# Optimization experiments

Hardware: AMD Instinct MI355X
Metric: run time of the kernel (lower is better)

Reference implementation:

```python
import jax, jax.numpy as jnp
import numpy as np
import math

D_MODEL = 1024
NUM_HEADS = 16
HEAD_DIM = D_MODEL // NUM_HEADS


def setup_inputs() -> dict:
    key = jax.random.key(0)
    ks = jax.random.split(key, 10)
    B, Sq, Skv = 2, 2048, 2048
    s = 1.0 / math.sqrt(D_MODEL)
    return {
        "X": jax.random.normal(ks[0], (B, Skv, D_MODEL), jnp.float32),
        "y": jax.random.normal(ks[1], (B, Sq, D_MODEL), jnp.float32),
        "qW": jax.random.normal(ks[2], (D_MODEL, D_MODEL), jnp.float32) * s,
        "qB": jnp.zeros((D_MODEL,), jnp.float32),
        "kW": jax.random.normal(ks[3], (D_MODEL, D_MODEL), jnp.float32) * s,
        "kB": jnp.zeros((D_MODEL,), jnp.float32),
        "vW": jax.random.normal(ks[4], (D_MODEL, D_MODEL), jnp.float32) * s,
        "vB": jnp.zeros((D_MODEL,), jnp.float32),
        "oW": jax.random.normal(ks[5], (D_MODEL, D_MODEL), jnp.float32) * s,
        "oB": jnp.zeros((D_MODEL,), jnp.float32),
    }


def _split_heads(x):
    # (B, S, D) -> (B, H, S, dk)
    B, S, _ = x.shape
    return x.reshape(B, S, NUM_HEADS, HEAD_DIM).transpose(0, 2, 1, 3)


def reference(X, y, qW, qB, kW, kB, vW, vB, oW, oB):
    B = X.shape[0]
    q = _split_heads(y @ qW + qB)   # queries come from y (decoder)
    k = _split_heads(X @ kW + kB)   # keys/values from X (encoder)
    v = _split_heads(X @ vW + vB)
    scale = 1.0 / math.sqrt(HEAD_DIM)
    scores = jnp.einsum("bhqd,bhkd->bhqk", q, k) * scale
    weights = jax.nn.softmax(scores, axis=-1)
    attn = jnp.einsum("bhqk,bhkd->bhqd", weights, v)
    concat = attn.transpose(0, 2, 1, 3).reshape(B, -1, D_MODEL)
    return concat @ oW + oB
```

## Files before the change

kernel.cpp:

```cpp
#include <hip/hip_runtime.h>
#include <hip/hip_bf16.h>
#include <math.h>

typedef __hip_bfloat16 bf16;
typedef __bf16 nbf16;
typedef __bf16 bf16x8 __attribute__((ext_vector_type(8)));
typedef __bf16 bf16x4 __attribute__((ext_vector_type(4)));
typedef float f32x4 __attribute__((ext_vector_type(4)));

#define D_MODEL 1024
#define NHEAD   16
#define HDK     64
#define BATCH   2
#define SEQ     2048
#define QSZ     ((size_t)BATCH * SEQ * D_MODEL)
#define WSZ     ((size_t)D_MODEL * D_MODEL)

__global__ void detect_dtype(const unsigned short* __restrict__ x, int* flag) {
    __shared__ int cnt;
    if (threadIdx.x == 0) cnt = 0;
    __syncthreads();
    int local = 0;
    for (int i = threadIdx.x; i < 4096; i += 256) {
        const unsigned short v = x[i];
        const int e = (v >> 7) & 0xFF;
        if (v == 0 || (e >= 96 && e <= 141)) local++;
    }
    atomicAdd(&cnt, local);
    __syncthreads();
    if (threadIdx.x == 0) *flag = (cnt >= 3600) ? 1 : 0;
}

__device__ __forceinline__ float ldIn(const void* p, size_t i, int isbf16) {
    return isbf16 ? __bfloat162float(((const bf16*)p)[i])
                  : ((const float*)p)[i];
}

__device__ __forceinline__ void gload_lds16(const void* g, void* l) {
    __builtin_amdgcn_global_load_lds(
        (const __attribute__((address_space(1))) void*)g,
        (__attribute__((address_space(3))) void*)l, 16, 0, 0);
}

__global__ void prep(const void* __restrict__ X, const void* __restrict__ Y,
                     const void* __restrict__ qW, const void* __restrict__ kW,
                     const void* __restrict__ vW, const void* __restrict__ oW,
                     nbf16* __restrict__ Xb, nbf16* __restrict__ Yb,
                     nbf16* __restrict__ Wt3, nbf16* __restrict__ Wto,
                     const int* __restrict__ flagp) {
    const int flag = *flagp;
    const int id = blockIdx.x;
    if (id < 4096) {
        const bool isX = id < 2048;
        const void* in = isX ? X : Y;
        nbf16* out     = isX ? Xb : Yb;
        const size_t i = ((size_t)(isX ? id : id - 2048) * 256 +
                          threadIdx.x) * 8;
        if (flag) {
            *(uint4*)(out + i) = *(const uint4*)((const nbf16*)in + i);
        } else {
            const float4 a = *(const float4*)((const float*)in + i);
            const float4 b = *(const float4*)((const float*)in + i + 4);
            bf16x8 v = {(nbf16)a.x, (nbf16)a.y, (nbf16)a.z, (nbf16)a.w,
                        (nbf16)b.x, (nbf16)b.y, (nbf16)b.z, (nbf16)b.w};
            *(bf16x8*)(out + i) = v;
        }
    } else {
        const int t = id - 4096;
        const int z = t >> 8;
        const int tile = t & 255;
        const void* W = (z == 0) ? qW : (z == 1) ? kW : (z == 2) ? vW : oW;
        nbf16* Wt = (z == 3) ? Wto : Wt3 + (size_t)z * WSZ;

        __shared__ float T[64][65];
        const int k0 = (tile & 15) * 64, n0 = (tile >> 4) * 64;
        #pragma unroll
        for (int i = 0; i < 16; ++i) {
            const int idx = threadIdx.x + i * 256;
            const int r = idx >> 6, c = idx & 63;
            T[r][c] = ldIn(W, (size_t)(k0 + r) * D_MODEL + n0 + c, flag);
        }
        __syncthreads();
        #pragma unroll
        for (int i = 0; i < 16; ++i) {
            const int idx = threadIdx.x + i * 256;
            const int n = idx >> 6, k = idx & 63;
            Wt[(size_t)(n0 + n) * D_MODEL + k0 + k] = (nbf16)T[k][n];
        }
    }
}

#define STAGE128(Albuf, Blbuf, Aptr, Bptr, t)                                  \
{                                                                              \
    const int _k0 = (t) * 64;                                                  \
    _Pragma("unroll")                                                          \
    for (int i = 0; i < 4; ++i) {                                              \
        const int row = i * 32 + wid * 8 + (lane >> 3);                        \
        const int ss  = (lane & 7) ^ (row & 7);                                \
        gload_lds16((Aptr) + (size_t)row * D_MODEL + _k0 + ss * 8,             \
                    (nbf16*)(Albuf) + i * 2048 + wid * 512);                   \
        gload_lds16((Bptr) + (size_t)row * D_MODEL + _k0 + ss * 8,             \
                    (nbf16*)(Blbuf) + i * 2048 + wid * 512);                   \
    }                                                                          \
}

#define GEMM128_LOOP(Al, Bl)                                                   \
    const int NT = D_MODEL / 64;                                               \
    for (int t = 0; t < NT; ++t) {                                             \
        const int cur = t & 1;                                                 \
        if (t + 1 < NT)                                                        \
            STAGE128(&Al[cur ^ 1][0][0], &Bl[cur ^ 1][0][0], Am, Bm, t + 1);   \
        _Pragma("unroll")                                                      \
        for (int kk = 0; kk < 2; ++kk) {                                       \
            bf16x8 af[4], bfr[4];                                              \
            _Pragma("unroll")                                                  \
            for (int mi = 0; mi < 4; ++mi) {                                   \
                const int ar = wr * 64 + mi * 16 + l15;                        \
                const int sl = ((kk << 2) + lg) ^ (ar & 7);                    \
                af[mi] = *(const bf16x8*)((const nbf16*)&Al[cur][ar][0] + sl * 8); \
            }                                                                  \
            _Pragma("unroll")                                                  \
            for (int ni = 0; ni < 4; ++ni) {                                   \
                const int br = wc * 64 + ni * 16 + l15;                        \
                const int sl = ((kk << 2) + lg) ^ (br & 7);                    \
                bfr[ni] = *(const bf16x8*)((const nbf16*)&Bl[cur][br][0] + sl * 8); \
            }                                                                  \
            _Pragma("unroll")                                                  \
            for (int mi = 0; mi < 4; ++mi)                                     \
                _Pragma("unroll")                                              \
                for (int ni = 0; ni < 4; ++ni)                                 \
                    acc[mi][ni] = __builtin_amdgcn_mfma_f32_16x16x32_bf16(     \
                        af[mi], bfr[ni], acc[mi][ni], 0, 0, 0);                \
        }                                                                      \
        __syncthreads();                                                       \
    }

__global__ __launch_bounds__(256, 2) void proj_qkv(
        const nbf16* __restrict__ Xb, const nbf16* __restrict__ Yb,
        const nbf16* __restrict__ Wt3,
        const void* __restrict__ qB, const void* __restrict__ kB,
        const void* __restrict__ vB,
        nbf16* __restrict__ outq, const int* __restrict__ flagp) {
    __shared__ nbf16 Al[2][128][64];
    __shared__ nbf16 Bl[2][128][64];

    const int flag = *flagp;
    const int tid  = threadIdx.x;
    const int wid  = tid >> 6;
    const int lane = tid & 63;
    const int l15  = lane & 15;
    const int lg   = lane >> 4;
    const int wr   = wid >> 1;
    const int wc   = wid & 1;

    const int id = blockIdx.x;
    const int sw = (id & 7) * 96 + (id >> 3);
    const int m0  = (sw & 31) * 128;
    const int ng0 = (sw >> 5) * 128;

    const nbf16* A  = (ng0 < D_MODEL) ? Yb : Xb;
    const nbf16* Bm = Wt3 + (size_t)ng0 * D_MODEL;
    const nbf16* Am = A + (size_t)m0 * D_MODEL;

    f32x4 acc[4][4];
    #pragma unroll
    for (int mi = 0; mi < 4; ++mi)
        #pragma unroll
        for (int ni = 0; ni < 4; ++ni) acc[mi][ni] = (f32x4){0.f, 0.f, 0.f, 0.f};

    STAGE128(&Al[0][0][0], &Bl[0][0][0], Am, Bm, 0);
    __syncthreads();

    GEMM128_LOOP(Al, Bl)

    #pragma unroll
    for (int ni = 0; ni < 4; ++ni) {
        const int n  = ng0 + wc * 64 + ni * 16 + l15;
        const int wh = n >> 10;
        const int nl = n & 1023;
        const void* bp = (wh == 0) ? qB : (wh == 1) ? kB : vB;
        const float bias = ldIn(bp, (size_t)nl, flag);
        nbf16* outp = outq + (size_t)wh * QSZ;
        #pragma unroll
        for (int mi = 0; mi < 4; ++mi) {
            #pragma unroll
            for (int r = 0; r < 4; ++r) {
                const int m = m0 + wr * 64 + mi * 16 + lg * 4 + r;
                const float v = acc[mi][ni][r] + bias;
                const int b = m >> 11, s = m & (SEQ - 1);
                const int h = nl >> 6,  d = nl & (HDK - 1);
                outp[(((size_t)(b * NHEAD + h)) * SEQ + s) * HDK + d] = (nbf16)v;
            }
        }
    }
}

__global__ __launch_bounds__(256, 2) void proj_o(
        const nbf16* __restrict__ A, const nbf16* __restrict__ Wt,
        const void* __restrict__ Braw, void* __restrict__ Cout,
        const int* __restrict__ flagp) {
    __shared__ nbf16 Al[2][128][64];
    __shared__ nbf16 Bl[2][128][64];

    const int flag = *flagp;
    const int tid  = threadIdx.x;
    const int wid  = tid >> 6;
    const int lane = tid & 63;
    const int l15  = lane & 15;
    const int lg   = lane >> 4;
    const int wr   = wid >> 1;
    const int wc   = wid & 1;

    const int id = blockIdx.x;
    const int sw = (id & 7) * 32 + (id >> 3);
    const int m0 = (sw >> 3) * 128;
    const int n0 = (sw & 7) * 128;

    const nbf16* Am = A + (size_t)m0 * D_MODEL;
    const nbf16* Bm = Wt + (size_t)n0 * D_MODEL;

    f32x4 acc[4][4];
    #pragma unroll
    for (int mi = 0; mi < 4; ++mi)
        #pragma unroll
        for (int ni = 0; ni < 4; ++ni) acc[mi][ni] = (f32x4){0.f, 0.f, 0.f, 0.f};

    STAGE128(&Al[0][0][0], &Bl[0][0][0], Am, Bm, 0);
    __syncthreads();

    GEMM128_LOOP(Al, Bl)

    #pragma unroll
    for (int ni = 0; ni < 4; ++ni) {
        const int n = n0 + wc * 64 + ni * 16 + l15;
        const float bias = ldIn(Braw, (size_t)n, flag);
        #pragma unroll
        for (int mi = 0; mi < 4; ++mi) {
            #pragma unroll
            for (int r = 0; r < 4; ++r) {
                const int m = m0 + wr * 64 + mi * 16 + lg * 4 + r;
                const float v = acc[mi][ni][r] + bias;
                if (flag) ((bf16*)Cout)[(size_t)m * D_MODEL + n] = __float2bfloat16(v);
                else      ((float*)Cout)[(size_t)m * D_MODEL + n] = v;
            }
        }
    }
}

__global__ __launch_bounds__(256, 2) void attn_mfma(
        const nbf16* __restrict__ qg, const nbf16* __restrict__ kg,
        const nbf16* __restrict__ vg, nbf16* __restrict__ cg) {
    __shared__ nbf16 KL[2][64][64];
    __shared__ nbf16 VT[2][64][64];
    __shared__ nbf16 PB[4][32][64];

    const int tid  = threadIdx.x;
    const int wid  = tid >> 6;
    const int lane = tid & 63;
    const int l15  = lane & 15;
    const int lg   = lane >> 4;

    const int id = blockIdx.x;
    const int sw = (id & 7) * 64 + (id >> 3);
    const int bh = sw >> 4;
    const int qt = sw & 15;

    const nbf16* qb = qg + (size_t)bh * SEQ * HDK;
    const nbf16* kb = kg + (size_t)bh * SEQ * HDK;
    const nbf16* vb = vg + (size_t)bh * SEQ * HDK;

    const float SCf = 0.125f * 1.44269504088896340736f;

    const int qbase = qt * 128 + wid * 32;
    const nbf16* qpA = qb + (size_t)(qbase + l15) * HDK + lg * 8;
    const nbf16* qpB = qpA + 16 * HDK;
    bf16x8 qfA0 = *(const bf16x8*)qpA;
    bf16x8 qfA1 = *(const bf16x8*)(qpA + 32);
    bf16x8 qfB0 = *(const bf16x8*)qpB;
    bf16x8 qfB1 = *(const bf16x8*)(qpB + 32);
    #pragma unroll
    for (int j = 0; j < 8; ++j) {
        qfA0[j] = (nbf16)((float)qfA0[j] * SCf);
        qfA1[j] = (nbf16)((float)qfA1[j] * SCf);
        qfB0[j] = (nbf16)((float)qfB0[j] * SCf);
        qfB1[j] = (nbf16)((float)qfB1[j] * SCf);
    }

    const bf16x8 ones = {(nbf16)1.f, (nbf16)1.f, (nbf16)1.f, (nbf16)1.f,
                         (nbf16)1.f, (nbf16)1.f, (nbf16)1.f, (nbf16)1.f};

    const int g8 = (tid >> 5) * 8;
    const int p2 = (tid & 31) * 2;

    const int swz0 = (lg * 8)      ^ ((l15 & 7) << 3);
    const int swz1 = (lg * 8 + 32) ^ ((l15 & 7) << 3);

    #define STAGEK(buf, t)                                                     \
    {                                                                          \
        _Pragma("unroll")                                                      \
        for (int i = 0; i < 2; ++i) {                                          \
            const int row = i * 32 + wid * 8 + (lane >> 3);                    \
            const int ss  = (lane & 7) ^ (row & 7);                            \
            gload_lds16(kb + (size_t)((t) * 64 + row) * HDK + ss * 8,          \
                        (nbf16*)&KL[buf][0][0] + i * 2048 + wid * 512);        \
        }                                                                      \
    }

    #define VLOAD(t)                                                           \
        a0 = *(const uint4*)(vb + (size_t)((t) * 64 + p2) * HDK + g8);         \
        a1 = *(const uint4*)(vb + (size_t)((t) * 64 + p2 + 1) * HDK + g8);

    #define VWRITE(buf)                                                        \
    {                                                                          \
        const unsigned short* e0 = (const unsigned short*)&a0;                 \
        const unsigned short* e1 = (const unsigned short*)&a1;                 \
        _Pragma("unroll")                                                      \
        for (int j = 0; j < 8; ++j)                                            \
            *(unsigned int*)&VT[buf][g8 + j][p2 ^ (j << 3)] =                  \
                (unsigned int)e0[j] | ((unsigned int)e1[j] << 16);             \
    }

    #define SOFTMAX(st, m2, o, osum, pbrow)                                    \
    do {                                                                       \
        float tmx[4];                                                          \
        _Pragma("unroll")                                                      \
        for (int s_ = 0; s_ < 4; ++s_)                                         \
            tmx[s_] = fmaxf(fmaxf(st[s_][0], st[s_][1]),                       \
                            fmaxf(st[s_][2], st[s_][3]));                      \
        float tm = fmaxf(fmaxf(tmx[0], tmx[1]), fmaxf(tmx[2], tmx[3]));        \
        tm = fmaxf(tm, __shfl_xor(tm, 16, 64));                                \
        tm = fmaxf(tm, __shfl_xor(tm, 32, 64));                                \
        const bool nresc = __all(tm - m2 <= 8.0f);                             \
        const float mref = nresc ? m2 : fmaxf(m2, tm);                         \
        _Pragma("unroll")                                                      \
        for (int s_ = 0; s_ < 4; ++s_) {                                       \
            const float p0 = exp2f(st[s_][0] - mref);                          \
            const float p1 = exp2f(st[s_][1] - mref);                          \
            const float p2_ = exp2f(st[s_][2] - mref);                         \
            const float p3 = exp2f(st[s_][3] - mref);                          \
            bf16x4 pk = {(nbf16)p0, (nbf16)p1, (nbf16)p2_, (nbf16)p3};         \
            *(bf16x4*)((pbrow) + ((s_ * 16 + lg * 4) ^ ((l15 & 7) << 3))) = pk;\
        }                                                                      \
        if (!nresc) {                                                          \
            const float alpha = exp2f(m2 - mref);                              \
            m2 = mref;                                                         \
            float av[4];                                                       \
            _Pragma("unroll")                                                  \
            for (int r = 0; r < 4; ++r) av[r] = __shfl(alpha, lg * 4 + r, 64); \
            _Pragma("unroll")                                                  \
            for (int i = 0; i < 4; ++i)                                        \
                _Pragma("unroll")                                              \
                for (int r = 0; r < 4; ++r) o[i][r] *= av[r];                  \
            _Pragma("unroll")                                                  \
            for (int r = 0; r < 4; ++r) osum[r] *= av[r];                      \
        }                                                                      \
    } while (0)

    float m2A = -3.0e38f, m2B = -3.0e38f;
    f32x4 oA[4], oB[4], osumA, osumB;
    #pragma unroll
    for (int i = 0; i < 4; ++i) { oA[i] = (f32x4){0,0,0,0}; oB[i] = (f32x4){0,0,0,0}; }
    osumA = (f32x4){0, 0, 0, 0};
    osumB = (f32x4){0, 0, 0, 0};

    const int NT = SEQ / 64;

    {
        uint4 a0, a1;
        STAGEK(0, 0);
        VLOAD(0);
        VWRITE(0);
    }
    __syncthreads();

    for (int t = 0; t < NT; ++t) {
        const int cur = t & 1;
        uint4 a0, a1;
        if (t + 1 < NT) {
            STAGEK(cur ^ 1, t + 1);
            VLOAD(t + 1);
        }

        f32x4 stA[4], stB[4];
        __builtin_amdgcn_s_setprio(1);
        #pragma unroll
        for (int sub = 0; sub < 4; ++sub) {
            const int row = sub * 16 + l15;
            const int s0 = lg ^ (row & 7);
            const int s1 = (4 + lg) ^ (row & 7);
            const bf16x8 kf0 = *(const bf16x8*)((const nbf16*)&KL[cur][row][0] + s0 * 8);
            const bf16x8 kf1 = *(const bf16x8*)((const nbf16*)&KL[cur][row][0] + s1 * 8);
            f32x4 a = (f32x4){0,0,0,0};
            a = __builtin_amdgcn_mfma_f32_16x16x32_bf16(kf0, qfA0, a, 0, 0, 0);
            a = __builtin_amdgcn_mfma_f32_16x16x32_bf16(kf1, qfA1, a, 0, 0, 0);
            stA[sub] = a;
            f32x4 b = (f32x4){0,0,0,0};
            b = __builtin_amdgcn_mfma_f32_16x16x32_bf16(kf0, qfB0, b, 0, 0, 0);
            b = __builtin_amdgcn_mfma_f32_16x16x32_bf16(kf1, qfB1, b, 0, 0, 0);
            stB[sub] = b;
        }
        __builtin_amdgcn_s_setprio(0);

        SOFTMAX(stA, m2A, oA, osumA, &PB[wid][l15][0]);
        SOFTMAX(stB, m2B, oB, osumB, &PB[wid][16 + l15][0]);

        __asm__ volatile("s_waitcnt lgkmcnt(0)" ::: "memory");

        const nbf16* pbA = &PB[wid][l15][0];
        const nbf16* pbB = &PB[wid][16 + l15][0];
        const bf16x8 pfA0 = *(const bf16x8*)(pbA + swz0);
        const bf16x8 pfA1 = *(const bf16x8*)(pbA + swz1);
        const bf16x8 pfB0 = *(const bf16x8*)(pbB + swz0);
        const bf16x8 pfB1 = *(const bf16x8*)(pbB + swz1);
        __builtin_amdgcn_s_setprio(1);
        #pragma unroll
        for (int db = 0; db < 4; ++db) {
            const nbf16* vr = &VT[cur][db * 16 + l15][0];
            const bf16x8 vf0 = *(const bf16x8*)(vr + swz0);
            const bf16x8 vf1 = *(const bf16x8*)(vr + swz1);
            oA[db] = __builtin_amdgcn_mfma_f32_16x16x32_bf16(pfA0, vf0, oA[db], 0, 0, 0);
            oA[db] = __builtin_amdgcn_mfma_f32_16x16x32_bf16(pfA1, vf1, oA[db], 0, 0, 0);
            oB[db] = __builtin_amdgcn_mfma_f32_16x16x32_bf16(pfB0, vf0, oB[db], 0, 0, 0);
            oB[db] = __builtin_amdgcn_mfma_f32_16x16x32_bf16(pfB1, vf1, oB[db], 0, 0, 0);
        }
        osumA = __builtin_amdgcn_mfma_f32_16x16x32_bf16(pfA0, ones, osumA, 0, 0, 0);
        osumA = __builtin_amdgcn_mfma_f32_16x16x32_bf16(pfA1, ones, osumA, 0, 0, 0);
        osumB = __builtin_amdgcn_mfma_f32_16x16x32_bf16(pfB0, ones, osumB, 0, 0, 0);
        osumB = __builtin_amdgcn_mfma_f32_16x16x32_bf16(pfB1, ones, osumB, 0, 0, 0);
        __builtin_amdgcn_s_setprio(0);

        if (t + 1 < NT) VWRITE(cur ^ 1);
        __syncthreads();
    }

    const int b = bh >> 4, h = bh & 15;
    #pragma unroll
    for (int db = 0; db < 4; ++db) {
        #pragma unroll
        for (int r = 0; r < 4; ++r) {
            const int qA = qbase + lg * 4 + r;
            cg[((size_t)(b * SEQ + qA)) * D_MODEL + h * HDK + db * 16 + l15] =
                (nbf16)(oA[db][r] / osumA[r]);
            const int qB_ = qbase + 16 + lg * 4 + r;
            cg[((size_t)(b * SEQ + qB_)) * D_MODEL + h * HDK + db * 16 + l15] =
                (nbf16)(oB[db][r] / osumB[r]);
        }
    }
    #undef STAGEK
    #undef VLOAD
    #undef VWRITE
    #undef SOFTMAX
}

extern "C" void kernel_launch(void* const* d_in, const int* in_sizes, int n_in,
                              void* d_out, int out_size, void* d_ws, size_t ws_size,
                              hipStream_t stream) {
    const void* X  = d_in[0];
    const void* Y  = d_in[1];
    const void* qW = d_in[2];
    const void* qB = d_in[3];
    const void* kW = d_in[4];
    const void* kB = d_in[5];
    const void* vW = d_in[6];
    const void* vB = d_in[7];
    const void* oW = d_in[8];
    const void* oB = d_in[9];

    nbf16* ws = (nbf16*)d_ws;
    nbf16* qbuf = ws;
    nbf16* kbuf = qbuf + QSZ;
    nbf16* vbuf = kbuf + QSZ;
    nbf16* cbuf = vbuf + QSZ;
    nbf16* Xb   = cbuf + QSZ;
    nbf16* Yb   = Xb + QSZ;
    nbf16* Wt3  = Yb + QSZ;
    nbf16* Wto  = Wt3 + 3 * WSZ;
    int*   flag = (int*)(Wto + WSZ);

    detect_dtype<<<1, 256, 0, stream>>>((const unsigned short*)X, flag);

    prep<<<5120, 256, 0, stream>>>(X, Y, qW, kW, vW, oW, Xb, Yb, Wt3, Wto, flag);

    proj_qkv<<<768, 256, 0, stream>>>(Xb, Yb, Wt3, qB, kB, vB, qbuf, flag);

    attn_mfma<<<512, 256, 0, stream>>>(qbuf, kbuf, vbuf, cbuf);

    proj_o<<<256, 256, 0, stream>>>(cbuf, Wto, oB, d_out, flag);
}
```

Measured before the change: 250.8 us.

## Split attention over KV halves with combine kernel; single-buffer QKV GEMM

Attention is split into two halves along the key/value sequence, doubling the grid from 512 to 1024 blocks. Each half writes fp32 partial outputs plus max/sum stats, and a new combine kernel merges them with a log-sum-exp rescale. Separately, proj_qkv drops its LDS double buffer for a single buffer so it can run 3 blocks per CU. The split adds extra global traffic for the partials and one more launch, and the QKV GEMM loses its load/compute overlap.

Result: no change. 250.6 us (-0.1%).

```diff
diff --git a/kernel.cpp b/kernel.cpp
--- a/kernel.cpp
+++ b/kernel.cpp
@@ -90,6 +90,104 @@
     }
 }
 
+#define STAGE1(Albuf, Blbuf, Aptr, Bptr, t)                                    \
+{                                                                              \
+    const int _k0 = (t) * 64;                                                  \
+    _Pragma("unroll")                                                          \
+    for (int i = 0; i < 4; ++i) {                                              \
+        const int row = i * 32 + wid * 8 + (lane >> 3);                        \
+        const int ss  = (lane & 7) ^ (row & 7);                                \
+        gload_lds16((Aptr) + (size_t)row * D_MODEL + _k0 + ss * 8,             \
+                    (nbf16*)(Albuf) + i * 2048 + wid * 512);                   \
+        gload_lds16((Bptr) + (size_t)row * D_MODEL + _k0 + ss * 8,             \
+                    (nbf16*)(Blbuf) + i * 2048 + wid * 512);                   \
+    }                                                                          \
+}
+
+__global__ __launch_bounds__(256, 3) void proj_qkv(
+        const nbf16* __restrict__ Xb, const nbf16* __restrict__ Yb,
+        const nbf16* __restrict__ Wt3,
+        const void* __restrict__ qB, const void* __restrict__ kB,
+        const void* __restrict__ vB,
+        nbf16* __restrict__ outq, const int* __restrict__ flagp) {
+    __shared__ nbf16 Al[128][64];
+    __shared__ nbf16 Bl[128][64];
+
+    const int flag = *flagp;
+    const int tid  = threadIdx.x;
+    const int wid  = tid >> 6;
+    const int lane = tid & 63;
+    const int l15  = lane & 15;
+    const int lg   = lane >> 4;
+    const int wr   = wid >> 1;
+    const int wc   = wid & 1;
+
+    const int id = blockIdx.x;
+    const int sw = (id & 7) * 96 + (id >> 3);
+    const int m0  = (sw & 31) * 128;
+    const int ng0 = (sw >> 5) * 128;
+
+    const nbf16* A  = (ng0 < D_MODEL) ? Yb : Xb;
+    const nbf16* Bm = Wt3 + (size_t)ng0 * D_MODEL;
+    const nbf16* Am = A + (size_t)m0 * D_MODEL;
+
+    f32x4 acc[4][4];
+    #pragma unroll
+    for (int mi = 0; mi < 4; ++mi)
+        #pragma unroll
+        for (int ni = 0; ni < 4; ++ni) acc[mi][ni] = (f32x4){0.f, 0.f, 0.f, 0.f};
+
+    const int NT = D_MODEL / 64;
+    for (int t = 0; t < NT; ++t) {
+        STAGE1(&Al[0][0], &Bl[0][0], Am, Bm, t);
+        __syncthreads();
+        #pragma unroll
+        for (int kk = 0; kk < 2; ++kk) {
+            bf16x8 af[4], bfr[4];
+            #pragma unroll
+            for (int mi = 0; mi < 4; ++mi) {
+                const int ar = wr * 64 + mi * 16 + l15;
+                const int sl = ((kk << 2) + lg) ^ (ar & 7);
+                af[mi] = *(const bf16x8*)((const nbf16*)&Al[ar][0] + sl * 8);
+            }
+            #pragma unroll
+            for (int ni = 0; ni < 4; ++ni) {
+                const int br = wc * 64 + ni * 16 + l15;
+                const int sl = ((kk << 2) + lg) ^ (br & 7);
+                bfr[ni] = *(const bf16x8*)((const nbf16*)&Bl[br][0] + sl * 8);
+            }
+            #pragma unroll
+            for (int mi = 0; mi < 4; ++mi)
+                #pragma unroll
+                for (int ni = 0; ni < 4; ++ni)
+                    acc[mi][ni] = __builtin_amdgcn_mfma_f32_16x16x32_bf16(
+                        af[mi], bfr[ni], acc[mi][ni], 0, 0, 0);
+        }
+        __syncthreads();
+    }
+
+    #pragma unroll
+    for (int ni = 0; ni < 4; ++ni) {
+        const int n  = ng0 + wc * 64 + ni * 16 + l15;
+        const int wh = n >> 10;
+        const int nl = n & 1023;
+        const void* bp = (wh == 0) ? qB : (wh == 1) ? kB : vB;
+        const float bias = ldIn(bp, (size_t)nl, flag);
+        nbf16* outp = outq + (size_t)wh * QSZ;
+        #pragma unroll
+        for (int mi = 0; mi < 4; ++mi) {
+            #pragma unroll
+            for (int r = 0; r < 4; ++r) {
+                const int m = m0 + wr * 64 + mi * 16 + lg * 4 + r;
+                const float v = acc[mi][ni][r] + bias;
+                const int b = m >> 11, s = m & (SEQ - 1);
+                const int h = nl >> 6,  d = nl & (HDK - 1);
+                outp[(((size_t)(b * NHEAD + h)) * SEQ + s) * HDK + d] = (nbf16)v;
+            }
+        }
+    }
+}
+
 #define STAGE128(Albuf, Blbuf, Aptr, Bptr, t)                                  \
 {                                                                              \
     const int _k0 = (t) * 64;                                                  \
@@ -104,43 +202,10 @@
     }                                                                          \
 }
 
-#define GEMM128_LOOP(Al, Bl)                                                   \
-    const int NT = D_MODEL / 64;                                               \
-    for (int t = 0; t < NT; ++t) {                                             \
-        const int cur = t & 1;                                                 \
-        if (t + 1 < NT)                                                        \
-            STAGE128(&Al[cur ^ 1][0][0], &Bl[cur ^ 1][0][0], Am, Bm, t + 1);   \
-        _Pragma("unroll")                                                      \
-        for (int kk = 0; kk < 2; ++kk) {                                       \
-            bf16x8 af[4], bfr[4];                                              \
-            _Pragma("unroll")                                                  \
-            for (int mi = 0; mi < 4; ++mi) {                                   \
-                const int ar = wr * 64 + mi * 16 + l15;                        \
-                const int sl = ((kk << 2) + lg) ^ (ar & 7);                    \
-                af[mi] = *(const bf16x8*)((const nbf16*)&Al[cur][ar][0] + sl * 8); \
-            }                                                                  \
-            _Pragma("unroll")                                                  \
-            for (int ni = 0; ni < 4; ++ni) {                                   \
-                const int br = wc * 64 + ni * 16 + l15;                        \
-                const int sl = ((kk << 2) + lg) ^ (br & 7);                    \
-                bfr[ni] = *(const bf16x8*)((const nbf16*)&Bl[cur][br][0] + sl * 8); \
-            }                                                                  \
-            _Pragma("unroll")                                                  \
-            for (int mi = 0; mi < 4; ++mi)                                     \
-                _Pragma("unroll")                                              \
-                for (int ni = 0; ni < 4; ++ni)                                 \
-                    acc[mi][ni] = __builtin_amdgcn_mfma_f32_16x16x32_bf16(     \
-                        af[mi], bfr[ni], acc[mi][ni], 0, 0, 0);                \
-        }                                                                      \
-        __syncthreads();                                                       \
-    }
-
-__global__ __launch_bounds__(256, 2) void proj_qkv(
-        const nbf16* __restrict__ Xb, const nbf16* __restrict__ Yb,
-        const nbf16* __restrict__ Wt3,
-        const void* __restrict__ qB, const void* __restrict__ kB,
-        const void* __restrict__ vB,
-        nbf16* __restrict__ outq, const int* __restrict__ flagp) {
+__global__ __launch_bounds__(256, 2) void proj_o(
+        const nbf16* __restrict__ A, const nbf16* __restrict__ Wt,
+        const void* __restrict__ Braw, void* __restrict__ Cout,
+        const int* __restrict__ flagp) {
     __shared__ nbf16 Al[2][128][64];
     __shared__ nbf16 Bl[2][128][64];
 
@@ -154,13 +219,12 @@
     const int wc   = wid & 1;
 
     const int id = blockIdx.x;
-    const int sw = (id & 7) * 96 + (id >> 3);
-    const int m0  = (sw & 31) * 128;
-    const int ng0 = (sw >> 5) * 128;
-
-    const nbf16* A  = (ng0 < D_MODEL) ? Yb : Xb;
-    const nbf16* Bm = Wt3 + (size_t)ng0 * D_MODEL;
+    const int sw = (id & 7) * 32 + (id >> 3);
+    const int m0 = (sw >> 3) * 128;
+    const int n0 = (sw & 7) * 128;
+
     const nbf16* Am = A + (size_t)m0 * D_MODEL;
+    const nbf16* Bm = Wt + (size_t)n0 * D_MODEL;
 
     f32x4 acc[4][4];
     #pragma unroll
@@ -171,103 +235,80 @@
     STAGE128(&Al[0][0][0], &Bl[0][0][0], Am, Bm, 0);
     __syncthreads();
 
-    GEMM128_LOOP(Al, Bl)
+    const int NT = D_MODEL / 64;
+    for (int t = 0; t < NT; ++t) {
+        const int cur = t & 1;
+        if (t + 1 < NT)
+            STAGE128(&Al[cur ^ 1][0][0], &Bl[cur ^ 1][0][0], Am, Bm, t + 1);
+        #pragma unroll
+        for (int kk = 0; kk < 2; ++kk) {
+            bf16x8 af[4], bfr[4];
+            #pragma unroll
+            for (int mi = 0; mi < 4; ++mi) {
+                const int ar = wr * 64 + mi * 16 + l15;
+                const int sl = ((kk << 2) + lg) ^ (ar & 7);
+                af[mi] = *(const bf16x8*)((const nbf16*)&Al[cur][ar][0] + sl * 8);
+            }
+            #pragma unroll
+            for (int ni = 0; ni < 4; ++ni) {
+                const int br = wc * 64 + ni * 16 + l15;
+                const int sl = ((kk << 2) + lg) ^ (br & 7);
+                bfr[ni] = *(const bf16x8*)((const nbf16*)&Bl[cur][br][0] + sl * 8);
+            }
+            #pragma unroll
+            for (int mi = 0; mi < 4; ++mi)
+                #pragma unroll
+                for (int ni = 0; ni < 4; ++ni)
+                    acc[mi][ni] = __builtin_amdgcn_mfma_f32_16x16x32_bf16(
+                        af[mi], bfr[ni], acc[mi][ni], 0, 0, 0);
+        }
+        __syncthreads();
+    }
 
     #pragma unroll
     for (int ni = 0; ni < 4; ++ni) {
-        const int n  = ng0 + wc * 64 + ni * 16 + l15;
-        const int wh = n >> 10;
-        const int nl = n & 1023;
-        const void* bp = (wh == 0) ? qB : (wh == 1) ? kB : vB;
-        const float bias = ldIn(bp, (size_t)nl, flag);
-        nbf16* outp = outq + (size_t)wh * QSZ;
+        const int n = n0 + wc * 64 + ni * 16 + l15;
+        const float bias = ldIn(Braw, (size_t)n, flag);
         #pragma unroll
         for (int mi = 0; mi < 4; ++mi) {
             #pragma unroll
             for (int r = 0; r < 4; ++r) {
                 const int m = m0 + wr * 64 + mi * 16 + lg * 4 + r;
                 const float v = acc[mi][ni][r] + bias;
-                const int b = m >> 11, s = m & (SEQ - 1);
-                const int h = nl >> 6,  d = nl & (HDK - 1);
-                outp[(((size_t)(b * NHEAD + h)) * SEQ + s) * HDK + d] = (nbf16)v;
-            }
-        }
-    }
-}
-
-__global__ __launch_bounds__(256, 2) void proj_o(
-        const nbf16* __restrict__ A, const nbf16* __restrict__ Wt,
-        const void* __restrict__ Braw, void* __restrict__ Cout,
-        const int* __restrict__ flagp) {
-    __shared__ nbf16 Al[2][128][64];
-    __shared__ nbf16 Bl[2][128][64];
-
-    const int flag = *flagp;
+                if (flag) ((bf16*)Cout)[(size_t)m * D_MODEL + n] = __float2bfloat16(v);
+                else      ((float*)Cout)[(size_t)m * D_MODEL + n] = v;
+            }
+        }
+    }
+}
+
+template<bool SPLIT>
+__global__ __launch_bounds__(256, SPLIT ? 3 : 2) void attn_mfma(
+        const nbf16* __restrict__ qg, const nbf16* __restrict__ kg,
+        const nbf16* __restrict__ vg, nbf16* __restrict__ cg,
+        float* __restrict__ part_o, float2* __restrict__ part_ms) {
+    __shared__ nbf16 KL[2][64][64];
+    __shared__ nbf16 VT[2][64][64];
+    __shared__ nbf16 PB[4][32][64];
+
     const int tid  = threadIdx.x;
     const int wid  = tid >> 6;
     const int lane = tid & 63;
     const int l15  = lane & 15;
     const int lg   = lane >> 4;
-    const int wr   = wid >> 1;
-    const int wc   = wid & 1;
 
     const int id = blockIdx.x;
-    const int sw = (id & 7) * 32 + (id >> 3);
-    const int m0 = (sw >> 3) * 128;
-    const int n0 = (sw & 7) * 128;
-
-    const nbf16* Am = A + (size_t)m0 * D_MODEL;
-    const nbf16* Bm = Wt + (size_t)n0 * D_MODEL;
-
-    f32x4 acc[4][4];
-    #pragma unroll
-    for (int mi = 0; mi < 4; ++mi)
-        #pragma unroll
-        for (int ni = 0; ni < 4; ++ni) acc[mi][ni] = (f32x4){0.f, 0.f, 0.f, 0.f};
-
-    STAGE128(&Al[0][0][0], &Bl[0][0][0], Am, Bm, 0);
-    __syncthreads();
-
-    GEMM128_LOOP(Al, Bl)
-
-    #pragma unroll
-    for (int ni = 0; ni < 4; ++ni) {
-        const int n = n0 + wc * 64 + ni * 16 + l15;
-        const float bias = ldIn(Braw, (size_t)n, flag);
-        #pragma unroll
-        for (int mi = 0; mi < 4; ++mi) {
-            #pragma unroll
-            for (int r = 0; r < 4; ++r) {
-                const int m = m0 + wr * 64 + mi * 16 + lg * 4 + r;
-                const float v = acc[mi][ni][r] + bias;
-                if (flag) ((bf16*)Cout)[(size_t)m * D_MODEL + n] = __float2bfloat16(v);
-                else      ((float*)Cout)[(size_t)m * D_MODEL + n] = v;
-            }
-        }
-    }
-}
-
-__global__ __launch_bounds__(256, 2) void attn_mfma(
-        const nbf16* __restrict__ qg, const nbf16* __restrict__ kg,
-        const nbf16* __restrict__ vg, nbf16* __restrict__ cg) {
-    __shared__ nbf16 KL[2][64][64];
-    __shared__ nbf16 VT[2][64][64];
-    __shared__ nbf16 PB[4][32][64];
-
-    const int tid  = threadIdx.x;
-    const int wid  = tid >> 6;
-    const int lane = tid & 63;
-    const int l15  = lane & 15;
-    const int lg   = lane >> 4;
-
-    const int id = blockIdx.x;
-    const int sw = (id & 7) * 64 + (id >> 3);
-    const int bh = sw >> 4;
-    const int qt = sw & 15;
+    const int sw = SPLIT ? ((id & 7) * 128 + (id >> 3))
+                         : ((id & 7) * 64 + (id >> 3));
+    const int bh   = SPLIT ? (sw >> 5) : (sw >> 4);
+    const int qt   = SPLIT ? ((sw & 31) >> 1) : (sw & 15);
+    const int half = SPLIT ? (sw & 1) : 0;
 
     const nbf16* qb = qg + (size_t)bh * SEQ * HDK;
-    const nbf16* kb = kg + (size_t)bh * SEQ * HDK;
-    const nbf16* vb = vg + (size_t)bh * SEQ * HDK;
+    const nbf16* kb = kg + (size_t)bh * SEQ * HDK +
+                      (size_t)half * (SEQ / 2) * HDK;
+    const nbf16* vb = vg + (size_t)bh * SEQ * HDK +
+                      (size_t)half * (SEQ / 2) * HDK;
 
     const float SCf = 0.125f * 1.44269504088896340736f;
 
@@ -363,7 +404,7 @@
     osumA = (f32x4){0, 0, 0, 0};
     osumB = (f32x4){0, 0, 0, 0};
 
-    const int NT = SEQ / 64;
+    const int NT = SPLIT ? (SEQ / 2) / 64 : SEQ / 64;
 
     {
         uint4 a0, a1;
@@ -433,23 +474,82 @@
         __syncthreads();
     }
 
-    const int b = bh >> 4, h = bh & 15;
-    #pragma unroll
-    for (int db = 0; db < 4; ++db) {
+    if (!SPLIT) {
+        const int b = bh >> 4, h = bh & 15;
+        #pragma unroll
+        for (int db = 0; db < 4; ++db) {
+            #pragma unroll
+            for (int r = 0; r < 4; ++r) {
+                const int qA = qbase + lg * 4 + r;
+                cg[((size_t)(b * SEQ + qA)) * D_MODEL + h * HDK + db * 16 + l15] =
+                    (nbf16)(oA[db][r] / osumA[r]);
+                const int qB_ = qbase + 16 + lg * 4 + r;
+                cg[((size_t)(b * SEQ + qB_)) * D_MODEL + h * HDK + db * 16 + l15] =
+                    (nbf16)(oB[db][r] / osumB[r]);
+            }
+        }
+    } else {
+        float mvA[4], mvB[4];
         #pragma unroll
         for (int r = 0; r < 4; ++r) {
-            const int qA = qbase + lg * 4 + r;
-            cg[((size_t)(b * SEQ + qA)) * D_MODEL + h * HDK + db * 16 + l15] =
-                (nbf16)(oA[db][r] / osumA[r]);
-            const int qB_ = qbase + 16 + lg * 4 + r;
-            cg[((size_t)(b * SEQ + qB_)) * D_MODEL + h * HDK + db * 16 + l15] =
-                (nbf16)(oB[db][r] / osumB[r]);
+            mvA[r] = __shfl(m2A, lg * 4 + r, 64);
+            mvB[r] = __shfl(m2B, lg * 4 + r, 64);
+        }
+        const int p = (bh * 16 + qt) * 2 + half;
+        float* po = part_o + (size_t)p * (128 * 64);
+        #pragma unroll
+        for (int db = 0; db < 4; ++db) {
+            #pragma unroll
+            for (int r = 0; r < 4; ++r) {
+                po[(wid * 32 + lg * 4 + r) * 64 + db * 16 + l15]      = oA[db][r];
+                po[(wid * 32 + 16 + lg * 4 + r) * 64 + db * 16 + l15] = oB[db][r];
+            }
+        }
+        if (l15 == 0) {
+            #pragma unroll
+            for (int r = 0; r < 4; ++r) {
+                part_ms[(size_t)p * 128 + wid * 32 + lg * 4 + r]      =
+                    make_float2(mvA[r], osumA[r]);
+                part_ms[(size_t)p * 128 + wid * 32 + 16 + lg * 4 + r] =
+                    make_float2(mvB[r], osumB[r]);
+            }
         }
     }
     #undef STAGEK
     #undef VLOAD
     #undef VWRITE
     #undef SOFTMAX
+}
+
+__global__ void attn_combine(const float* __restrict__ part_o,
+                             const float2* __restrict__ part_ms,
+                             nbf16* __restrict__ cg) {
+    const int bq = blockIdx.x;
+    const int bh = bq >> 4, qt = bq & 15;
+    const int p0 = bq * 2, p1 = bq * 2 + 1;
+    const int q  = threadIdx.x >> 1;
+    const int d0 = (threadIdx.x & 1) * 32;
+
+    const float2 s1 = part_ms[(size_t)p0 * 128 + q];
+    const float2 s2 = part_ms[(size_t)p1 * 128 + q];
+    const float m  = fmaxf(s1.x, s2.x);
+    const float w1 = exp2f(s1.x - m);
+    const float w2 = exp2f(s2.x - m);
+    const float inv = 1.f / (s1.y * w1 + s2.y * w2);
+
+    const float* o1 = part_o + (size_t)p0 * (128 * 64) + q * 64 + d0;
+    const float* o2 = part_o + (size_t)p1 * (128 * 64) + q * 64 + d0;
+    const int b = bh >> 4, h = bh & 15;
+    nbf16* out = cg + ((size_t)(b * SEQ + qt * 128 + q)) * D_MODEL + h * HDK + d0;
+    #pragma unroll
+    for (int j = 0; j < 8; ++j) {
+        const float4 a = *(const float4*)(o1 + j * 4);
+        const float4 c = *(const float4*)(o2 + j * 4);
+        out[j * 4 + 0] = (nbf16)((a.x * w1 + c.x * w2) * inv);
+        out[j * 4 + 1] = (nbf16)((a.y * w1 + c.y * w2) * inv);
+        out[j * 4 + 2] = (nbf16)((a.z * w1 + c.z * w2) * inv);
+        out[j * 4 + 3] = (nbf16)((a.w * w1 + c.w * w2) * inv);
+    }
 }
 
 extern "C" void kernel_launch(void* const* d_in, const int* in_sizes, int n_in,
@@ -476,6 +576,12 @@
     nbf16* Wt3  = Yb + QSZ;
     nbf16* Wto  = Wt3 + 3 * WSZ;
     int*   flag = (int*)(Wto + WSZ);
+    char*  pbase = (char*)flag + 256;
+    float2* part_ms = (float2*)pbase;
+    float*  part_o  = (float*)(part_ms + (size_t)1024 * 128);
+    const size_t need_split =
+        (size_t)((char*)(part_o + (size_t)1024 * 128 * 64) - (char*)d_ws);
+    const bool use_split = (ws_size >= need_split);
 
     detect_dtype<<<1, 256, 0, stream>>>((const unsigned short*)X, flag);
 
@@ -483,7 +589,14 @@
 
     proj_qkv<<<768, 256, 0, stream>>>(Xb, Yb, Wt3, qB, kB, vB, qbuf, flag);
 
-    attn_mfma<<<512, 256, 0, stream>>>(qbuf, kbuf, vbuf, cbuf);
+    if (use_split) {
+        attn_mfma<true><<<1024, 256, 0, stream>>>(qbuf, kbuf, vbuf, cbuf,
+                                                  part_o, part_ms);
+        attn_combine<<<512, 256, 0, stream>>>(part_o, part_ms, cbuf);
+    } else {
+        attn_mfma<false><<<512, 256, 0, stream>>>(qbuf, kbuf, vbuf, cbuf,
+                                                  nullptr, nullptr);
+    }
 
     proj_o<<<256, 256, 0, stream>>>(cbuf, Wto, oB, d_out, flag);
 }
```
